# Performance work log

Measured on AMD Instinct MI355X. Metric: run time of the kernel, lower is better.

Reference implementation:

```python
import jax, jax.numpy as jnp
import numpy as np


def setup_inputs() -> dict:
    key = jax.random.key(0)
    N, E, D, NF, V = 50000, 600000, 128, 3, 8  # nodes, edges, embed_dim, edge feat cols, vocab
    ks = jax.random.split(key, 6)
    nfeat = jax.random.normal(ks[0], (N, D), jnp.float32)
    src = jax.random.randint(ks[1], (E,), 0, N)
    dst = jax.random.randint(ks[2], (E,), 0, N)
    efeat_idx = jax.random.randint(ks[3], (E, NF), 0, V)
    edge_emb = jax.random.normal(ks[4], (NF, V, D), jnp.float32) * 0.02  # OGB bond-encoder tables
    W = jax.random.normal(ks[5], (D, D), jnp.float32) / np.sqrt(D)
    b = jnp.zeros((D,), jnp.float32)
    return {"nfeat": nfeat, "src": src, "dst": dst, "efeat_idx": efeat_idx,
            "edge_emb": edge_emb, "W": W, "b": b}


def reference(nfeat, src, dst, efeat_idx, edge_emb, W, b):
    N, D = nfeat.shape
    NF = edge_emb.shape[0]
    # OGB_EdgeEncoder: sum of per-column categorical embedding lookups -> [E, D]
    efeat = edge_emb[jnp.arange(NF)[None, :], efeat_idx].sum(axis=1)
    # u_add_e message: gather src node feats, add projected edge feats -> [E, D]
    m = nfeat[src] + efeat
    # sum aggregation onto destination nodes
    neigh = jax.ops.segment_sum(m, dst, num_segments=N)
    # in-degree + 1 normalization
    degs = jax.ops.segment_sum(jnp.ones_like(dst, jnp.float32), dst, num_segments=N) + 1.0
    # (nfeat + neigh) / degs, then linear projection
    return ((nfeat + neigh) / degs[:, None]) @ W + b
```

## Files before the change

### kernel.cpp

```cpp
#include <hip/hip_runtime.h>

#define D  128
#define NF 3
#define V  8

typedef __attribute__((ext_vector_type(8))) short short8;
typedef __attribute__((ext_vector_type(4))) float f32x4;

__device__ inline unsigned short f2bf(float x) {
    unsigned u = __builtin_bit_cast(unsigned, x);
    return (unsigned short)((u + 0x7FFFu + ((u >> 16) & 1u)) >> 16);
}
__device__ inline float bflo(unsigned u) {
    return __builtin_bit_cast(float, u << 16);
}
__device__ inline float bfhi(unsigned u) {
    return __builtin_bit_cast(float, u & 0xFFFF0000u);
}


__global__ __launch_bounds__(256) void build_kernel(
    const int* __restrict__ src, const int* __restrict__ dst,
    const int* __restrict__ eidx, const float* __restrict__ emb,
    const float* __restrict__ Wm, const float* __restrict__ nfeat,
    int* __restrict__ count, unsigned* __restrict__ packed,
    unsigned short* __restrict__ Tb, unsigned short* __restrict__ WB,
    unsigned* __restrict__ nfb32, int E, int eb, int N, int nfb_blocks)
{
    int b = blockIdx.x, t = threadIdx.x;
    if (b < eb) {
        int e = b * 256 + t;
        if (e < E) {
            int d = dst[e];
            int r = atomicAdd(&count[d], 1);
            int i0 = eidx[e * NF + 0];
            int i1 = eidx[e * NF + 1];
            int i2 = eidx[e * NF + 2];
            if (r < 64)
                packed[(size_t)d * 64 + r] =
                    (unsigned)src[e]
                  | ((unsigned)(i0 + (i1 << 3) + (i2 << 6)) << 16);
        }
    } else if (b < eb + 257) {
        int tid = (b - eb) * 256 + t;
        if (tid < 513 * 128) {
            int cmb = tid >> 7, c = tid & 127;
            float s = 0.0f;
            if (cmb < 512) {
                s = emb[(cmb & 7) * D + c]
                  + emb[(V + ((cmb >> 3) & 7)) * D + c]
                  + emb[(2 * V + (cmb >> 6)) * D + c];
            }
            Tb[tid] = f2bf(s);
        }
    } else if (b < eb + 321) {
        int tid = (b - (eb + 257)) * 256 + t;
        int j = tid & 7, lane = (tid >> 3) & 63, ks = (tid >> 9) & 3, n = tid >> 11;
        int k = ks * 32 + ((lane >> 4) << 3) + j;
        int c = n * 16 + (lane & 15);
        WB[tid] = f2bf(Wm[k * D + c]);
    } else if (b < eb + 321 + nfb_blocks) {
        int tid = (b - (eb + 321)) * 256 + t;
        float4 v = ((const float4*)nfeat)[tid];
        nfb32[tid * 2 + 0] = (unsigned)f2bf(v.x) | ((unsigned)f2bf(v.y) << 16);
        nfb32[tid * 2 + 1] = (unsigned)f2bf(v.z) | ((unsigned)f2bf(v.w) << 16);
    } else {
        if (t < 32) {
            nfb32[(size_t)N * 64 + 2 * t + 0] = 0u;
            nfb32[(size_t)N * 64 + 2 * t + 1] = 0u;
        }
    }
}


__device__ __attribute__((always_inline)) inline void grp8(
    const unsigned* __restrict__ nfb32, const unsigned* __restrict__ Tb32,
    unsigned rec, int j, int lane, float2& acc)
{
    unsigned u[8];
#pragma unroll
    for (int q = 0; q < 8; ++q) u[q] = (unsigned)__shfl((int)rec, j + q);
    unsigned av[8], tv[8];
#pragma unroll
    for (int q = 0; q < 8; ++q) {
        av[q] = nfb32[(u[q] & 0xFFFFu) * 64 + lane];
        tv[q] = Tb32[(u[q] >> 16) * 64 + lane];
    }
    float p0 = bflo(av[0]) + bflo(tv[0]);
    float p1 = bflo(av[1]) + bflo(tv[1]);
    float p2 = bflo(av[2]) + bflo(tv[2]);
    float p3 = bflo(av[3]) + bflo(tv[3]);
    float p4 = bflo(av[4]) + bflo(tv[4]);
    float p5 = bflo(av[5]) + bflo(tv[5]);
    float p6 = bflo(av[6]) + bflo(tv[6]);
    float p7 = bflo(av[7]) + bflo(tv[7]);
    acc.x += ((p0 + p1) + (p2 + p3)) + ((p4 + p5) + (p6 + p7));
    float q0 = bfhi(av[0]) + bfhi(tv[0]);
    float q1 = bfhi(av[1]) + bfhi(tv[1]);
    float q2 = bfhi(av[2]) + bfhi(tv[2]);
    float q3 = bfhi(av[3]) + bfhi(tv[3]);
    float q4 = bfhi(av[4]) + bfhi(tv[4]);
    float q5 = bfhi(av[5]) + bfhi(tv[5]);
    float q6 = bfhi(av[6]) + bfhi(tv[6]);
    float q7 = bfhi(av[7]) + bfhi(tv[7]);
    acc.y += ((q0 + q1) + (q2 + q3)) + ((q4 + q5) + (q6 + q7));
}


__global__ __launch_bounds__(1024) void fused_gp(
    const unsigned* __restrict__ nfb32,
    const unsigned* __restrict__ Tb32,
    const unsigned* __restrict__ packed,
    const int* __restrict__ count,
    const unsigned short* __restrict__ WB,
    const float* __restrict__ bias,
    float* __restrict__ out, int N)
{
    __shared__ unsigned short hA[16][136];
    int t = threadIdx.x, w = t >> 6, lane = t & 63;
    int quad = lane >> 4, l15 = lane & 15;
    int row0 = blockIdx.x * 16;
    int n = row0 + w;
    const unsigned SENT = (unsigned)N | (512u << 16);

    unsigned rec = SENT;
    int cnt = 0;
    unsigned sw = 0u;
    if (n < N) {
        rec = packed[(size_t)n * 64 + lane];
        cnt = count[n];
        sw = nfb32[(size_t)n * 64 + lane];
    }
    cnt = (cnt < 64) ? cnt : 64;
    rec = (lane < cnt) ? rec : SENT;

    float2 acc;
    acc.x = bflo(sw);
    acc.y = bfhi(sw);

    for (int j = 0; j < cnt; j += 8)
        grp8(nfb32, Tb32, rec, j, lane, acc);

    if (n < N) {
        float inv = 1.0f / (float)(cnt + 1);
        acc.x *= inv; acc.y *= inv;
        *(unsigned*)&hA[w][2 * lane] =
            (unsigned)f2bf(acc.x) | ((unsigned)f2bf(acc.y) << 16);
    }
    __syncthreads();

    if (w < 8) {
        short8 a[4];
#pragma unroll
        for (int ks = 0; ks < 4; ++ks)
            a[ks] = *(const short8*)&hA[l15][ks * 32 + quad * 8];

        f32x4 acc2 = {0.0f, 0.0f, 0.0f, 0.0f};
#pragma unroll
        for (int ks = 0; ks < 4; ++ks) {
            short8 bfr = *(const short8*)&WB[((w * 4 + ks) * 64 + lane) * 8];
            acc2 = __builtin_amdgcn_mfma_f32_16x16x32_bf16(a[ks], bfr, acc2, 0, 0, 0);
        }
        float bv = bias[w * 16 + l15];
        int col = w * 16 + l15;
#pragma unroll
        for (int rg = 0; rg < 4; ++rg) {
            int row = row0 + quad * 4 + rg;
            if (row < N) out[row * D + col] = acc2[rg] + bv;
        }
    }
}

extern "C" void kernel_launch(void* const* d_in, const int* in_sizes, int n_in,
                              void* d_out, int out_size, void* d_ws, size_t ws_size,
                              hipStream_t stream)
{
    const float* nfeat = (const float*)d_in[0];
    const int*   src   = (const int*)  d_in[1];
    const int*   dst   = (const int*)  d_in[2];
    const int*   eidx  = (const int*)  d_in[3];
    const float* emb   = (const float*)d_in[4];
    const float* Wm    = (const float*)d_in[5];
    const float* bias  = (const float*)d_in[6];
    float* out = (float*)d_out;

    int N = in_sizes[0] / D;
    int E = in_sizes[1];
    int eb = (E + 255) / 256;

    int* count = (int*)d_ws;
    unsigned* packed = (unsigned*)(count + N);
    unsigned short* Tb = (unsigned short*)(packed + (size_t)N * 64);
    unsigned short* WB = Tb + 513 * 128;
    unsigned* nfb32 = (unsigned*)(WB + 16384);

    hipMemsetAsync(count, 0, (size_t)N * sizeof(int), stream);

    int nfb_blocks = (N * D / 4 + 255) / 256;
    build_kernel<<<eb + 322 + nfb_blocks, 256, 0, stream>>>(
        src, dst, eidx, emb, Wm, nfeat, count, packed, Tb, WB, nfb32,
        E, eb, N, nfb_blocks);
    fused_gp<<<(N + 15) / 16, 1024, 0, stream>>>(
        nfb32, (const unsigned*)Tb, packed, count,
        WB, bias, out, N);
}
```

Before: 163.2 us.

## Split fused gather+projection into separate gather and projection kernels

The fused kernel, which ran 1024-thread blocks where half the waves sat idle during the MFMA projection, is split in two. A 256-thread gather kernel handles one node per wave and writes bf16 aggregated rows to a workspace buffer. A separate 512-thread projection kernel then loads 16 rows into LDS and runs the MFMA matmul. The aim is better occupancy and load balance in the gather phase, paid for by an extra global write/read of the N×128 bf16 intermediate and one more launch.

```diff
diff --git a/kernel.cpp b/kernel.cpp
--- a/kernel.cpp
+++ b/kernel.cpp
@@ -107,11 +107,40 @@
 }
 
 
-__global__ __launch_bounds__(1024) void fused_gp(
+__global__ __launch_bounds__(256) void gather_kernel(
     const unsigned* __restrict__ nfb32,
     const unsigned* __restrict__ Tb32,
     const unsigned* __restrict__ packed,
     const int* __restrict__ count,
+    unsigned* __restrict__ hout, int N)
+{
+    int t = threadIdx.x, w = t >> 6, lane = t & 63;
+    int n = blockIdx.x * 4 + w;
+    if (n >= N) return;
+    const unsigned SENT = (unsigned)N | (512u << 16);
+
+    unsigned rec = packed[(size_t)n * 64 + lane];
+    int cnt = count[n];
+    unsigned sw = nfb32[(size_t)n * 64 + lane];
+    cnt = (cnt < 64) ? cnt : 64;
+    rec = (lane < cnt) ? rec : SENT;
+
+    float2 acc;
+    acc.x = bflo(sw);
+    acc.y = bfhi(sw);
+
+    for (int j = 0; j < cnt; j += 8)
+        grp8(nfb32, Tb32, rec, j, lane, acc);
+
+    float inv = 1.0f / (float)(cnt + 1);
+    acc.x *= inv; acc.y *= inv;
+    hout[(size_t)n * 64 + lane] =
+        (unsigned)f2bf(acc.x) | ((unsigned)f2bf(acc.y) << 16);
+}
+
+
+__global__ __launch_bounds__(512) void proj_kernel(
+    const unsigned* __restrict__ h,
     const unsigned short* __restrict__ WB,
     const float* __restrict__ bias,
     float* __restrict__ out, int N)
@@ -120,54 +149,34 @@
     int t = threadIdx.x, w = t >> 6, lane = t & 63;
     int quad = lane >> 4, l15 = lane & 15;
     int row0 = blockIdx.x * 16;
-    int n = row0 + w;
-    const unsigned SENT = (unsigned)N | (512u << 16);
-
-    unsigned rec = SENT;
-    int cnt = 0;
-    unsigned sw = 0u;
-    if (n < N) {
-        rec = packed[(size_t)n * 64 + lane];
-        cnt = count[n];
-        sw = nfb32[(size_t)n * 64 + lane];
-    }
-    cnt = (cnt < 64) ? cnt : 64;
-    rec = (lane < cnt) ? rec : SENT;
-
-    float2 acc;
-    acc.x = bflo(sw);
-    acc.y = bfhi(sw);
-
-    for (int j = 0; j < cnt; j += 8)
-        grp8(nfb32, Tb32, rec, j, lane, acc);
-
-    if (n < N) {
-        float inv = 1.0f / (float)(cnt + 1);
-        acc.x *= inv; acc.y *= inv;
-        *(unsigned*)&hA[w][2 * lane] =
-            (unsigned)f2bf(acc.x) | ((unsigned)f2bf(acc.y) << 16);
+
+    {
+        int r = t >> 5;
+        int c = (t & 31) * 2;
+        uint2 v; v.x = 0u; v.y = 0u;
+        int row = row0 + r;
+        if (row < N) v = *(const uint2*)&h[(size_t)row * 64 + c];
+        *(uint2*)&hA[r][2 * c] = v;
     }
     __syncthreads();
 
-    if (w < 8) {
-        short8 a[4];
-#pragma unroll
-        for (int ks = 0; ks < 4; ++ks)
-            a[ks] = *(const short8*)&hA[l15][ks * 32 + quad * 8];
-
-        f32x4 acc2 = {0.0f, 0.0f, 0.0f, 0.0f};
-#pragma unroll
-        for (int ks = 0; ks < 4; ++ks) {
-            short8 bfr = *(const short8*)&WB[((w * 4 + ks) * 64 + lane) * 8];
-            acc2 = __builtin_amdgcn_mfma_f32_16x16x32_bf16(a[ks], bfr, acc2, 0, 0, 0);
-        }
-        float bv = bias[w * 16 + l15];
-        int col = w * 16 + l15;
-#pragma unroll
-        for (int rg = 0; rg < 4; ++rg) {
-            int row = row0 + quad * 4 + rg;
-            if (row < N) out[row * D + col] = acc2[rg] + bv;
-        }
+    short8 a[4];
+#pragma unroll
+    for (int ks = 0; ks < 4; ++ks)
+        a[ks] = *(const short8*)&hA[l15][ks * 32 + quad * 8];
+
+    f32x4 acc2 = {0.0f, 0.0f, 0.0f, 0.0f};
+#pragma unroll
+    for (int ks = 0; ks < 4; ++ks) {
+        short8 bfr = *(const short8*)&WB[((w * 4 + ks) * 64 + lane) * 8];
+        acc2 = __builtin_amdgcn_mfma_f32_16x16x32_bf16(a[ks], bfr, acc2, 0, 0, 0);
+    }
+    float bv = bias[w * 16 + l15];
+    int col = w * 16 + l15;
+#pragma unroll
+    for (int rg = 0; rg < 4; ++rg) {
+        int row = row0 + quad * 4 + rg;
+        if (row < N) out[row * D + col] = acc2[rg] + bv;
     }
 }
 
@@ -193,6 +202,7 @@
     unsigned short* Tb = (unsigned short*)(packed + (size_t)N * 64);
     unsigned short* WB = Tb + 513 * 128;
     unsigned* nfb32 = (unsigned*)(WB + 16384);
+    unsigned* hbuf = nfb32 + (size_t)(N + 1) * 64;
 
     hipMemsetAsync(count, 0, (size_t)N * sizeof(int), stream);
 
@@ -200,7 +210,8 @@
     build_kernel<<<eb + 322 + nfb_blocks, 256, 0, stream>>>(
         src, dst, eidx, emb, Wm, nfeat, count, packed, Tb, WB, nfb32,
         E, eb, N, nfb_blocks);
-    fused_gp<<<(N + 15) / 16, 1024, 0, stream>>>(
-        nfb32, (const unsigned*)Tb, packed, count,
-        WB, bias, out, N);
-}
+    gather_kernel<<<(N + 3) / 4, 256, 0, stream>>>(
+        nfb32, (const unsigned*)Tb, packed, count, hbuf, N);
+    proj_kernel<<<(N + 15) / 16, 512, 0, stream>>>(
+        hbuf, WB, bias, out, N);
+}
```

After: 165.1 us. About the same (+1.2%).

## Process four nodes per wave and 32 rows per block in fused gather-GEMM

Applied to the files above, without the earlier changes.

The fused gather/projection kernel now uses 512-thread blocks of 8 waves covering 32 nodes. Each wave aggregates 4 nodes in turn, and all 8 waves then run two MFMA tiles that share the same W fragment. Previously half the waves sat idle during the GEMM phase and each W fragment served only one 16-row tile. The trade-off is that gathers within a wave are now serialized across its 4 nodes, which lowers memory-level parallelism per wave and may hurt latency hiding in this gather-bound phase.

```diff
diff --git a/kernel.cpp b/kernel.cpp
--- a/kernel.cpp
+++ b/kernel.cpp
@@ -107,7 +107,7 @@
 }
 
 
-__global__ __launch_bounds__(1024) void fused_gp(
+__global__ __launch_bounds__(512) void fused_gp(
     const unsigned* __restrict__ nfb32,
     const unsigned* __restrict__ Tb32,
     const unsigned* __restrict__ packed,
@@ -116,58 +116,69 @@
     const float* __restrict__ bias,
     float* __restrict__ out, int N)
 {
-    __shared__ unsigned short hA[16][136];
+    __shared__ unsigned short hA[32][136];
     int t = threadIdx.x, w = t >> 6, lane = t & 63;
     int quad = lane >> 4, l15 = lane & 15;
-    int row0 = blockIdx.x * 16;
-    int n = row0 + w;
+    int row0 = blockIdx.x * 32;
+    int nb = row0 + 4 * w;
     const unsigned SENT = (unsigned)N | (512u << 16);
 
-    unsigned rec = SENT;
-    int cnt = 0;
-    unsigned sw = 0u;
-    if (n < N) {
-        rec = packed[(size_t)n * 64 + lane];
-        cnt = count[n];
-        sw = nfb32[(size_t)n * 64 + lane];
-    }
-    cnt = (cnt < 64) ? cnt : 64;
-    rec = (lane < cnt) ? rec : SENT;
-
-    float2 acc;
-    acc.x = bflo(sw);
-    acc.y = bfhi(sw);
-
-    for (int j = 0; j < cnt; j += 8)
-        grp8(nfb32, Tb32, rec, j, lane, acc);
-
-    if (n < N) {
-        float inv = 1.0f / (float)(cnt + 1);
-        acc.x *= inv; acc.y *= inv;
-        *(unsigned*)&hA[w][2 * lane] =
-            (unsigned)f2bf(acc.x) | ((unsigned)f2bf(acc.y) << 16);
+    unsigned rec[4], sw[4];
+    int cnt[4];
+#pragma unroll
+    for (int i = 0; i < 4; ++i) {
+        int n = nb + i;
+        if (n < N) {
+            rec[i] = packed[(size_t)n * 64 + lane];
+            cnt[i] = count[n];
+            sw[i]  = nfb32[(size_t)n * 64 + lane];
+        } else {
+            rec[i] = SENT; cnt[i] = 0; sw[i] = 0u;
+        }
+    }
+#pragma unroll
+    for (int i = 0; i < 4; ++i) {
+        cnt[i] = (cnt[i] < 64) ? cnt[i] : 64;
+        rec[i] = (lane < cnt[i]) ? rec[i] : SENT;
+    }
+
+#pragma unroll
+    for (int i = 0; i < 4; ++i) {
+        float2 acc; acc.x = bflo(sw[i]); acc.y = bfhi(sw[i]);
+        for (int j = 0; j < cnt[i]; j += 8)
+            grp8(nfb32, Tb32, rec[i], j, lane, acc);
+        if (nb + i < N) {
+            float inv = 1.0f / (float)(cnt[i] + 1);
+            acc.x *= inv; acc.y *= inv;
+            *(unsigned*)&hA[4 * w + i][2 * lane] =
+                (unsigned)f2bf(acc.x) | ((unsigned)f2bf(acc.y) << 16);
+        }
     }
     __syncthreads();
 
-    if (w < 8) {
-        short8 a[4];
-#pragma unroll
-        for (int ks = 0; ks < 4; ++ks)
-            a[ks] = *(const short8*)&hA[l15][ks * 32 + quad * 8];
-
-        f32x4 acc2 = {0.0f, 0.0f, 0.0f, 0.0f};
-#pragma unroll
-        for (int ks = 0; ks < 4; ++ks) {
-            short8 bfr = *(const short8*)&WB[((w * 4 + ks) * 64 + lane) * 8];
-            acc2 = __builtin_amdgcn_mfma_f32_16x16x32_bf16(a[ks], bfr, acc2, 0, 0, 0);
-        }
-        float bv = bias[w * 16 + l15];
-        int col = w * 16 + l15;
-#pragma unroll
-        for (int rg = 0; rg < 4; ++rg) {
-            int row = row0 + quad * 4 + rg;
-            if (row < N) out[row * D + col] = acc2[rg] + bv;
-        }
+    short8 a0[4], a1[4];
+#pragma unroll
+    for (int ks = 0; ks < 4; ++ks) {
+        a0[ks] = *(const short8*)&hA[l15][ks * 32 + quad * 8];
+        a1[ks] = *(const short8*)&hA[16 + l15][ks * 32 + quad * 8];
+    }
+
+    f32x4 acc0 = {0.0f, 0.0f, 0.0f, 0.0f};
+    f32x4 acc1 = {0.0f, 0.0f, 0.0f, 0.0f};
+#pragma unroll
+    for (int ks = 0; ks < 4; ++ks) {
+        short8 bfr = *(const short8*)&WB[((w * 4 + ks) * 64 + lane) * 8];
+        acc0 = __builtin_amdgcn_mfma_f32_16x16x32_bf16(a0[ks], bfr, acc0, 0, 0, 0);
+        acc1 = __builtin_amdgcn_mfma_f32_16x16x32_bf16(a1[ks], bfr, acc1, 0, 0, 0);
+    }
+    float bv = bias[w * 16 + l15];
+    int col = w * 16 + l15;
+#pragma unroll
+    for (int rg = 0; rg < 4; ++rg) {
+        int row = row0 + quad * 4 + rg;
+        if (row < N) out[row * D + col] = acc0[rg] + bv;
+        int row2 = row + 16;
+        if (row2 < N) out[row2 * D + col] = acc1[rg] + bv;
     }
 }
 
@@ -200,7 +211,7 @@
     build_kernel<<<eb + 322 + nfb_blocks, 256, 0, stream>>>(
         src, dst, eidx, emb, Wm, nfeat, count, packed, Tb, WB, nfb32,
         E, eb, N, nfb_blocks);
-    fused_gp<<<(N + 15) / 16, 1024, 0, stream>>>(
+    fused_gp<<<(N + 31) / 32, 512, 0, stream>>>(
         nfb32, (const unsigned*)Tb, packed, count,
         WB, bias, out, N);
 }
```

New measurement: 163.5 us. No clear change (+0.2%).
